# Kernel optimization log

Measured on AMD Instinct MI355X. Metric: run time of the kernel, lower is better.

The kernel has to match this reference:

```python
import jax, jax.numpy as jnp
import numpy as np

DIM = 1024
NUM_HEADS = 8
HEAD_DIM = 64
INNER = NUM_HEADS * HEAD_DIM  # 512


def setup_inputs() -> dict:
    key = jax.random.key(0)
    ks = jax.random.split(key, 7)
    B, N, M = 8, 512, 4096
    x = jax.random.normal(ks[0], (B, N, DIM), dtype=jnp.float32)
    context = jax.random.normal(ks[1], (B, M, DIM), dtype=jnp.float32)
    s_in = 1.0 / np.sqrt(DIM)
    s_inner = 1.0 / np.sqrt(INNER)
    # Linear weights stored as [in, out] for x @ W
    Wq = jax.random.normal(ks[2], (DIM, INNER), dtype=jnp.float32) * s_in
    Wk = jax.random.normal(ks[3], (DIM, INNER), dtype=jnp.float32) * s_in
    Wv = jax.random.normal(ks[4], (DIM, INNER), dtype=jnp.float32) * s_in
    Wo = jax.random.normal(ks[5], (INNER, DIM), dtype=jnp.float32) * s_inner
    bo = jax.random.normal(ks[6], (DIM,), dtype=jnp.float32) * 0.01
    return {"x": x, "context": context, "Wq": Wq, "Wk": Wk, "Wv": Wv, "Wo": Wo, "bo": bo}


def reference(x, context, Wq, Wk, Wv, Wo, bo):
    B, N, _ = x.shape
    M = context.shape[1]
    scale = HEAD_DIM ** -0.5
    # project and split heads: [B, H, N, D]
    q = (x @ Wq).reshape(B, N, NUM_HEADS, HEAD_DIM).transpose(0, 2, 1, 3)
    k = (context @ Wk).reshape(B, M, NUM_HEADS, HEAD_DIM).transpose(0, 2, 1, 3)
    v = (context @ Wv).reshape(B, M, NUM_HEADS, HEAD_DIM).transpose(0, 2, 1, 3)
    # full attention matrix [B, H, N, M] as in the original module
    attn = jax.nn.softmax(jnp.einsum('bhnd,bhmd->bhnm', q, k) * scale, axis=-1)
    out = jnp.einsum('bhnm,bhmd->bhnd', attn, v)  # [B, H, N, D]
    out = out.transpose(0, 2, 1, 3).reshape(B, N, INNER)
    return out @ Wo + bo
```

## Files before the change

kernel.cpp:

```cpp
#include <hip/hip_runtime.h>
#include <hip/hip_bf16.h>

#define B_SZ 8
#define N_Q 512
#define M_KV 4096
#define DIM 1024
#define INNER 512
#define NHEADS 8
#define HDIM 64

typedef __attribute__((ext_vector_type(4))) float floatx4;
typedef __attribute__((ext_vector_type(8))) short shortx8;
typedef __attribute__((ext_vector_type(4))) short shortx4;

__device__ inline unsigned short f2bf(float f) {
  union { float f; unsigned u; } x; x.f = f;
  unsigned r = x.u + 0x7FFFu + ((x.u >> 16) & 1u);
  return (unsigned short)(r >> 16);
}

__device__ inline shortx8 cvt8(floatx4 a, floatx4 b) {
  shortx8 h;
  h[0] = (short)f2bf(a[0]); h[1] = (short)f2bf(a[1]);
  h[2] = (short)f2bf(a[2]); h[3] = (short)f2bf(a[3]);
  h[4] = (short)f2bf(b[0]); h[5] = (short)f2bf(b[1]);
  h[6] = (short)f2bf(b[2]); h[7] = (short)f2bf(b[3]);
  return h;
}

__device__ inline void gload16(const void* g, void* l) {
  __builtin_amdgcn_global_load_lds(
      (const __attribute__((address_space(1))) void*)g,
      (__attribute__((address_space(3))) void*)l, 16, 0, 0);
}

__global__ void k_cvt_bf16(const float* __restrict__ src,
                           unsigned short* __restrict__ dst, long n) {
  long stride = (long)gridDim.x * 256 * 8;
  for (long i = ((long)blockIdx.x * 256 + threadIdx.x) * 8; i < n; i += stride) {
    floatx4 a = *reinterpret_cast<const floatx4*>(src + i);
    floatx4 b = *reinterpret_cast<const floatx4*>(src + i + 4);
    *reinterpret_cast<shortx8*>(dst + i) = cvt8(a, b);
  }
}

__global__ void k_transpose_all(const float* __restrict__ Wq,
                                const float* __restrict__ Wk,
                                const float* __restrict__ Wv,
                                const float* __restrict__ Wo,
                                unsigned short* __restrict__ Wqt,
                                unsigned short* __restrict__ Wkvt,
                                unsigned short* __restrict__ Wot) {
  __shared__ unsigned short t[32][36];
  const int z = blockIdx.z;
  const float* W;
  unsigned short* Wt;
  int K, N;
  if (z == 0)      { W = Wq; Wt = Wqt;  K = 1024; N = 512; }
  else if (z == 1) { W = Wk; Wt = Wkvt; K = 1024; N = 512; }
  else if (z == 2) { W = Wv; Wt = Wkvt + (size_t)512 * 1024; K = 1024; N = 512; }
  else             { W = Wo; Wt = Wot;  K = 512;  N = 1024; }
  if ((int)blockIdx.x * 32 >= K || (int)blockIdx.y * 32 >= N) return;
  const int kt = blockIdx.x * 32, nt = blockIdx.y * 32;
  const int tr = threadIdx.x >> 3;
  const int tc = (threadIdx.x & 7) * 4;
  floatx4 v = *reinterpret_cast<const floatx4*>(&W[(long)(kt + tr) * N + nt + tc]);
  #pragma unroll
  for (int j = 0; j < 4; ++j) t[tr][tc + j] = f2bf(v[j]);
  __syncthreads();
  shortx4 o;
  #pragma unroll
  for (int j = 0; j < 4; ++j) o[j] = (short)t[tc + j][tr];
  *reinterpret_cast<shortx4*>(&Wt[(long)(nt + tr) * K + kt + tc]) = o;
}

__global__ __launch_bounds__(256, 4)
void k_gemm_kv(const unsigned short* __restrict__ Ah,
               const unsigned short* __restrict__ Wkvt,
               unsigned short* __restrict__ Kh,
               unsigned short* __restrict__ Vt) {
  __shared__ unsigned short As[2][128 * 32];
  __shared__ unsigned short Bs[2][128 * 32];
  const int tid = threadIdx.x;
  const int lane = tid & 63;
  const int w = tid >> 6;
  const int wr = w >> 1, wc = w & 1;
  const int fr = lane & 15, fc = lane >> 4;

  const int L = ((blockIdx.x & 7) << 8) + (blockIdx.x >> 3);
  const int mt = L >> 3, nt = L & 7;
  const long arow0 = (long)mt << 7;
  const long bcol0 = (long)nt << 7;

  const int grow = lane >> 2;
  const int gpos = lane & 3;

  floatx4 acc[4][4] = {};

  #define STAGE(buf, kt)                                                      \
    {                                                                         \
      _Pragma("unroll")                                                       \
      for (int g = 0; g < 2; ++g) {                                           \
        const int rl = w * 32 + g * 16 + grow;                                \
        const int cc = gpos ^ ((rl >> 1) & 3);                                \
        gload16(Ah + (arow0 + rl) * 1024 + (kt) + cc * 8,                     \
                &As[buf][(w * 32 + g * 16) * 32]);                            \
        gload16(Wkvt + (bcol0 + rl) * 1024 + (kt) + cc * 8,                   \
                &Bs[buf][(w * 32 + g * 16) * 32]);                            \
      }                                                                       \
    }

  STAGE(0, 0);
  __syncthreads();

  for (int i = 0; i < 32; ++i) {
    const int cur = i & 1;
    if (i < 31) STAGE(cur ^ 1, (i + 1) << 5);

    shortx8 af[4], bf[4];
    #pragma unroll
    for (int rb = 0; rb < 4; ++rb) {
      int row = wr * 64 + rb * 16 + fr;
      af[rb] = *reinterpret_cast<const shortx8*>(
          &As[cur][row * 32 + ((fc ^ ((row >> 1) & 3)) * 8)]);
    }
    #pragma unroll
    for (int cb = 0; cb < 4; ++cb) {
      int row = wc * 64 + cb * 16 + fr;
      bf[cb] = *reinterpret_cast<const shortx8*>(
          &Bs[cur][row * 32 + ((fc ^ ((row >> 1) & 3)) * 8)]);
    }
    __builtin_amdgcn_s_setprio(1);
    #pragma unroll
    for (int rb = 0; rb < 4; ++rb) {
      #pragma unroll
      for (int cb = 0; cb < 4; ++cb)
        acc[rb][cb] = __builtin_amdgcn_mfma_f32_16x16x32_bf16(
            af[rb], bf[cb], acc[rb][cb], 0, 0, 0);
    }
    __builtin_amdgcn_s_setprio(0);
    __syncthreads();
  }
  #undef STAGE

  #pragma unroll
  for (int rb = 0; rb < 4; ++rb) {
    #pragma unroll
    for (int cb = 0; cb < 4; ++cb) {
      long gr0 = arow0 + wr * 64 + rb * 16 + fc * 4;
      long gc = bcol0 + wc * 64 + cb * 16 + fr;
      long b = gr0 >> 12, m = gr0 & 4095;
      if (gc < 512) {
        long h = gc >> 6, d = gc & 63;
        #pragma unroll
        for (int r = 0; r < 4; ++r)
          Kh[((((b * 8 + h) << 12) + m + r) << 6) + d] = f2bf(acc[rb][cb][r]);
      } else {
        long h = (gc - 512) >> 6, d = (gc - 512) & 63;
        shortx4 hv;
        #pragma unroll
        for (int r = 0; r < 4; ++r) hv[r] = (short)f2bf(acc[rb][cb][r]);
        *reinterpret_cast<shortx4*>(&Vt[(((b * 8 + h) * 64 + d) << 12) + m]) = hv;
      }
    }
  }
}

template<int MODE, bool ABF, int NCOL, int MBITS>
__global__ __launch_bounds__(512, 4)
void k_gemm(const void* __restrict__ Ap, const unsigned short* __restrict__ Bt,
            void* __restrict__ Cout, const float* __restrict__ bias,
            int M, int N, int K, float oscale) {
  __shared__ unsigned short As[2][128 * 32];
  __shared__ unsigned short Bs[2][256 * 32];
  const int tid = threadIdx.x;
  const int lane = tid & 63;
  const int w = tid >> 6;
  const int wr = w >> 2, wc = w & 3;

  const int cpx = gridDim.x >> 3;
  const int L = (blockIdx.x & 7) * cpx + (blockIdx.x >> 3);
  const long arow0 = (long)(L / NCOL) * 128;
  const long bcol0 = (long)(L % NCOL) * 256;

  const float* Af = (const float*)Ap;
  const unsigned short* Ah = (const unsigned short*)Ap;

  const int lsub = lane >> 2;
  const int lchunk = (lane & 3) ^ ((lane >> 3) & 3);
  const long brow0 = bcol0 + (w * 2 + 0) * 16 + lsub;
  const long brow1 = bcol0 + (w * 2 + 1) * 16 + lsub;
  const long ahrow = arow0 + w * 16 + lsub;
  const int arow = tid >> 2;
  const int acseg = tid & 3;
  const int aswz = arow * 32 + ((acseg ^ ((arow >> 1) & 3)) * 8);

  floatx4 acc[4][4] = {};

  #define STAGE_B(buf, kt)                                                   \
    {                                                                        \
      gload16(Bt + brow0 * K + (kt) + lchunk * 8, &Bs[buf][(w * 2) * 512]);  \
      gload16(Bt + brow1 * K + (kt) + lchunk * 8,                            \
              &Bs[buf][(w * 2 + 1) * 512]);                                  \
    }
  #define STAGE_AH(buf, kt) \
    gload16(Ah + ahrow * K + (kt) + lchunk * 8, &As[buf][w * 512]);

  if (ABF) {
    STAGE_AH(0, 0);
  } else {
    const float* src = Af + (arow0 + arow) * (long)K + acseg * 8;
    floatx4 a0 = *reinterpret_cast<const floatx4*>(src);
    floatx4 a1 = *reinterpret_cast<const floatx4*>(src + 4);
    *reinterpret_cast<shortx8*>(&As[0][aswz]) = cvt8(a0, a1);
  }
  STAGE_B(0, 0);
  __syncthreads();

  const int NK = K >> 5;
  for (int i = 0; i < NK; ++i) {
    const int cur = i & 1;
    const bool more = (i + 1) < NK;
    floatx4 a0, a1;
    if (more) {
      const long ktn = (long)(i + 1) << 5;
      if (ABF) {
        STAGE_AH(cur ^ 1, ktn);
      } else {
        const float* src = Af + (arow0 + arow) * (long)K + ktn + acseg * 8;
        a0 = *reinterpret_cast<const floatx4*>(src);
        a1 = *reinterpret_cast<const floatx4*>(src + 4);
      }
      STAGE_B(cur ^ 1, ktn);
    }

    shortx8 af[4], bf[4];
    #pragma unroll
    for (int rb = 0; rb < 4; ++rb) {
      int row = wr * 64 + rb * 16 + (lane & 15);
      af[rb] = *reinterpret_cast<const shortx8*>(
          &As[cur][row * 32 + (((lane >> 4) ^ ((row >> 1) & 3)) * 8)]);
    }
    #pragma unroll
    for (int cb = 0; cb < 4; ++cb) {
      int row = wc * 64 + cb * 16 + (lane & 15);
      bf[cb] = *reinterpret_cast<const shortx8*>(
          &Bs[cur][row * 32 + (((lane >> 4) ^ ((row >> 1) & 3)) * 8)]);
    }
    #pragma unroll
    for (int rb = 0; rb < 4; ++rb) {
      #pragma unroll
      for (int cb = 0; cb < 4; ++cb)
        acc[rb][cb] = __builtin_amdgcn_mfma_f32_16x16x32_bf16(
            af[rb], bf[cb], acc[rb][cb], 0, 0, 0);
    }

    if (more && !ABF)
      *reinterpret_cast<shortx8*>(&As[cur ^ 1][aswz]) = cvt8(a0, a1);
    __syncthreads();
  }
  #undef STAGE_B
  #undef STAGE_AH

  #pragma unroll
  for (int rb = 0; rb < 4; ++rb) {
    #pragma unroll
    for (int cb = 0; cb < 4; ++cb) {
      long gr0 = arow0 + wr * 64 + rb * 16 + (lane >> 4) * 4;
      long gc  = bcol0 + wc * 64 + cb * 16 + (lane & 15);
      if (MODE == 0) {
        float bv = bias[gc];
        #pragma unroll
        for (int r = 0; r < 4; ++r)
          ((float*)Cout)[(gr0 + r) * N + gc] = acc[rb][cb][r] + bv;
      } else if (MODE == 2) {
        long b = gr0 >> MBITS, m = gr0 & ((1 << MBITS) - 1);
        long h = gc >> 6, d = gc & 63;
        #pragma unroll
        for (int r = 0; r < 4; ++r)
          ((unsigned short*)Cout)[((((b * 8 + h) << MBITS) + m + r) << 6) + d] =
              f2bf(acc[rb][cb][r] * oscale);
      }
    }
  }
}

__global__ __launch_bounds__(256, 3)
void k_attn(const unsigned short* __restrict__ Qh,
            const unsigned short* __restrict__ Kh,
            const unsigned short* __restrict__ Vt,
            float* __restrict__ Opart, float* __restrict__ Lpart) {
  __shared__ unsigned short Qs[64 * 64];
  __shared__ unsigned short Ks[2][64 * 64];
  __shared__ unsigned short Vs[2][64 * 64];
  __shared__ unsigned short Ps[64][72];
  const int tid = threadIdx.x;
  const int lane = tid & 63;
  const int w = tid >> 6;
  const int wg = blockIdx.x;
  const int bh = wg & 63;
  const int qt = (wg >> 6) & 7;
  const int sp = wg >> 9;
  const int fr = lane & 15, fc = lane >> 4;

  const unsigned short* Qbase = Qh + (((long)bh << 9) + qt * 64) * 64;
  const unsigned short* Kbase = Kh + (((long)bh) << 18);
  const unsigned short* Vbase = Vt + (((long)bh) << 18);

  const int grow = lane >> 3;
  const int gpos = lane & 7;

  #define STAGE_KV(buf, mt_)                                              \
    { _Pragma("unroll")                                                   \
      for (int j = 0; j < 2; ++j) {                                       \
        const int r = w * 16 + j * 8 + grow;                              \
        const int c = gpos ^ (r & 7);                                     \
        gload16(Kbase + ((mt_) * 64 + r) * 64 + c * 8,                    \
                &Ks[buf][(w * 16 + j * 8) * 64]);                         \
        gload16(Vbase + (((long)r) << 12) + (mt_) * 64 + c * 8,           \
                &Vs[buf][(w * 16 + j * 8) * 64]);                         \
      } }

  const int mt0 = sp * 32;
  {
    #pragma unroll
    for (int j = 0; j < 2; ++j) {
      const int r = w * 16 + j * 8 + grow;
      const int c = gpos ^ (r & 7);
      gload16(Qbase + r * 64 + c * 8, &Qs[(w * 16 + j * 8) * 64]);
    }
    STAGE_KV(0, mt0);
  }
  __syncthreads();

  shortx8 qf[2];
  #pragma unroll
  for (int kk = 0; kk < 2; ++kk)
    qf[kk] = *reinterpret_cast<const shortx8*>(
        &Qs[(w * 16 + fr) * 64 + (((kk * 4 + fc) ^ (fr & 7)) * 8)]);

  floatx4 o_acc[4] = {};
  float l_part[4] = {0.f, 0.f, 0.f, 0.f};

  for (int it = 0; it < 32; ++it) {
    const int cur = it & 1;
    if (it < 31) STAGE_KV(cur ^ 1, mt0 + it + 1);

    floatx4 s[4];
    __builtin_amdgcn_s_setprio(1);
    #pragma unroll
    for (int cb = 0; cb < 4; ++cb) {
      int row = cb * 16 + fr;
      shortx8 k0 = *reinterpret_cast<const shortx8*>(
          &Ks[cur][row * 64 + ((fc ^ (fr & 7)) * 8)]);
      shortx8 k1 = *reinterpret_cast<const shortx8*>(
          &Ks[cur][row * 64 + (((4 + fc) ^ (fr & 7)) * 8)]);
      floatx4 z = {};
      z = __builtin_amdgcn_mfma_f32_16x16x32_bf16(qf[0], k0, z, 0, 0, 0);
      s[cb] = __builtin_amdgcn_mfma_f32_16x16x32_bf16(qf[1], k1, z, 0, 0, 0);
    }
    __builtin_amdgcn_s_setprio(0);

    #pragma unroll
    for (int cb = 0; cb < 4; ++cb) {
      #pragma unroll
      for (int r = 0; r < 4; ++r) {
        float pv = __expf(s[cb][r]);
        l_part[r] += pv;
        Ps[w * 16 + fc * 4 + r][cb * 16 + fr] = f2bf(pv);
      }
    }

    __builtin_amdgcn_s_setprio(1);
    #pragma unroll
    for (int kk = 0; kk < 2; ++kk) {
      shortx8 pf = *reinterpret_cast<const shortx8*>(
          &Ps[w * 16 + fr][kk * 32 + fc * 8]);
      #pragma unroll
      for (int db = 0; db < 4; ++db) {
        int row = db * 16 + fr;
        shortx8 vf = *reinterpret_cast<const shortx8*>(
            &Vs[cur][row * 64 + (((kk * 4 + fc) ^ (fr & 7)) * 8)]);
        o_acc[db] = __builtin_amdgcn_mfma_f32_16x16x32_bf16(
            pf, vf, o_acc[db], 0, 0, 0);
      }
    }
    __builtin_amdgcn_s_setprio(0);
    __syncthreads();
  }
  #undef STAGE_KV

  #pragma unroll
  for (int r = 0; r < 4; ++r) {
    float l = l_part[r];
    l += __shfl_xor(l, 1);
    l += __shfl_xor(l, 2);
    l += __shfl_xor(l, 4);
    l += __shfl_xor(l, 8);
    l_part[r] = l;
  }
  float* Ob = Opart + (long)wg * 4096;
  #pragma unroll
  for (int db = 0; db < 4; ++db) {
    #pragma unroll
    for (int r = 0; r < 4; ++r)
      Ob[(w * 16 + fc * 4 + r) * 64 + db * 16 + fr] = o_acc[db][r];
  }
  if (fr == 0) {
    #pragma unroll
    for (int r = 0; r < 4; ++r)
      Lpart[(long)wg * 64 + w * 16 + fc * 4 + r] = l_part[r];
  }
}

__global__ void k_attn_reduce(const float* __restrict__ Opart,
                              const float* __restrict__ Lpart,
                              unsigned short* __restrict__ Aat) {
  const int tid = threadIdx.x;
  const int g = blockIdx.x * 4 + (tid >> 6);
  const int d = tid & 63;
  const int bh = g >> 9, n = g & 511;
  const int b = bh >> 3, h = bh & 7;
  const int qt = n >> 6, rr = n & 63;
  const long i0 = ((long)(qt * 64 + bh)) * 4096 + rr * 64 + d;
  const long i1 = ((long)(512 + qt * 64 + bh)) * 4096 + rr * 64 + d;
  const float l = Lpart[(long)(qt * 64 + bh) * 64 + rr] +
                  Lpart[(long)(512 + qt * 64 + bh) * 64 + rr];
  const float o = Opart[i0] + Opart[i1];
  Aat[((long)(b * 512 + n)) * 512 + h * 64 + d] = f2bf(o / l);
}

extern "C" void kernel_launch(void* const* d_in, const int* in_sizes, int n_in,
                              void* d_out, int out_size, void* d_ws, size_t ws_size,
                              hipStream_t stream) {
  const float* x   = (const float*)d_in[0];
  const float* ctx = (const float*)d_in[1];
  const float* Wq  = (const float*)d_in[2];
  const float* Wk  = (const float*)d_in[3];
  const float* Wv  = (const float*)d_in[4];
  const float* Wo  = (const float*)d_in[5];
  const float* bo  = (const float*)d_in[6];
  float* out = (float*)d_out;

  char* ws = (char*)d_ws;
  unsigned short* Qh   = (unsigned short*)(ws);
  unsigned short* Kh   = (unsigned short*)(ws + (4ull  << 20));
  unsigned short* Vt   = (unsigned short*)(ws + (36ull << 20));
  unsigned short* ctxh = (unsigned short*)(ws + (68ull << 20));
  unsigned short* Aat  = (unsigned short*)(ws + (68ull << 20));
  float*          Opart= (float*)         (ws + (76ull << 20));
  float*          Lpart= (float*)         (ws + (92ull << 20));
  unsigned short* Wqt  = (unsigned short*)(ws + (132ull << 20));
  unsigned short* Wkvt = (unsigned short*)(ws + (133ull << 20));
  unsigned short* Wot  = (unsigned short*)(ws + (135ull << 20));

  k_cvt_bf16<<<dim3(2048), dim3(256), 0, stream>>>(
      ctx, ctxh, (long)B_SZ * M_KV * DIM);

  k_transpose_all<<<dim3(32, 32, 4), dim3(256), 0, stream>>>(
      Wq, Wk, Wv, Wo, Wqt, Wkvt, Wot);

  k_gemm<2, false, 2, 9><<<dim3(64), dim3(512), 0, stream>>>(
      x, Wqt, Qh, nullptr, B_SZ * N_Q, INNER, DIM, 0.125f);

  k_gemm_kv<<<dim3(2048), dim3(256), 0, stream>>>(ctxh, Wkvt, Kh, Vt);

  k_attn<<<dim3(1024), dim3(256), 0, stream>>>(Qh, Kh, Vt, Opart, Lpart);
  k_attn_reduce<<<dim3(8192), dim3(256), 0, stream>>>(Opart, Lpart, Aat);

  k_gemm<0, true, 4, 0><<<dim3(128), dim3(512), 0, stream>>>(
      Aat, Wot, out, bo, B_SZ * N_Q, DIM, INNER, 1.0f);
}
```

Baseline: 259.1 us.

## Fuse Q projection into KV GEMM, widen attention tiles, retile output GEMM

```diff
diff --git a/kernel.cpp b/kernel.cpp
--- a/kernel.cpp
+++ b/kernel.cpp
@@ -12,6 +12,8 @@
 typedef __attribute__((ext_vector_type(4))) float floatx4;
 typedef __attribute__((ext_vector_type(8))) short shortx8;
 typedef __attribute__((ext_vector_type(4))) short shortx4;
+
+#define QSCALE 0.18033688011112042f
 
 __device__ inline unsigned short f2bf(float f) {
   union { float f; unsigned u; } x; x.f = f;
@@ -75,47 +77,96 @@
 }
 
 __global__ __launch_bounds__(256, 4)
-void k_gemm_kv(const unsigned short* __restrict__ Ah,
-               const unsigned short* __restrict__ Wkvt,
-               unsigned short* __restrict__ Kh,
-               unsigned short* __restrict__ Vt) {
-  __shared__ unsigned short As[2][128 * 32];
-  __shared__ unsigned short Bs[2][128 * 32];
+void k_proj(const unsigned short* __restrict__ ctxh,
+            const float* __restrict__ x,
+            const unsigned short* __restrict__ Wkvt,
+            const unsigned short* __restrict__ Wqt,
+            unsigned short* __restrict__ Kh,
+            unsigned short* __restrict__ Vt,
+            unsigned short* __restrict__ Qh) {
+  __shared__ unsigned short As[2][4096];
+  __shared__ unsigned short Bs[2][4096];
   const int tid = threadIdx.x;
   const int lane = tid & 63;
   const int w = tid >> 6;
   const int wr = w >> 1, wc = w & 1;
   const int fr = lane & 15, fc = lane >> 4;
-
-  const int L = ((blockIdx.x & 7) << 8) + (blockIdx.x >> 3);
-  const int mt = L >> 3, nt = L & 7;
-  const long arow0 = (long)mt << 7;
-  const long bcol0 = (long)nt << 7;
+  const bool isQ = (int)blockIdx.x >= 2048;
+
+  long arow0, bcol0;
+  const unsigned short* Bb;
+  if (!isQ) {
+    const int L = ((blockIdx.x & 7) << 8) + (blockIdx.x >> 3);
+    arow0 = (long)(L >> 3) << 7;
+    bcol0 = (long)(L & 7) << 7;
+    Bb = Wkvt;
+  } else {
+    const int t = blockIdx.x - 2048;
+    arow0 = (long)(t >> 2) << 7;
+    bcol0 = (long)(t & 3) << 7;
+    Bb = Wqt;
+  }
 
   const int grow = lane >> 2;
   const int gpos = lane & 3;
+  const int arw = tid >> 1;
+  const int ahalf = tid & 1;
+  const int aswz = (arw >> 1) & 3;
+  const int as0 = ((2 * ahalf) ^ aswz) * 8;
+  const int as1 = ((2 * ahalf + 1) ^ aswz) * 8;
 
   floatx4 acc[4][4] = {};
 
-  #define STAGE(buf, kt)                                                      \
-    {                                                                         \
-      _Pragma("unroll")                                                       \
+  #define STAGE_A(buf, kt)                                                    \
+    { _Pragma("unroll")                                                       \
       for (int g = 0; g < 2; ++g) {                                           \
         const int rl = w * 32 + g * 16 + grow;                                \
         const int cc = gpos ^ ((rl >> 1) & 3);                                \
-        gload16(Ah + (arow0 + rl) * 1024 + (kt) + cc * 8,                     \
+        gload16(ctxh + (arow0 + rl) * 1024 + (kt) + cc * 8,                   \
                 &As[buf][(w * 32 + g * 16) * 32]);                            \
-        gload16(Wkvt + (bcol0 + rl) * 1024 + (kt) + cc * 8,                   \
+      } }
+  #define STAGE_B(buf, kt)                                                    \
+    { _Pragma("unroll")                                                       \
+      for (int g = 0; g < 2; ++g) {                                           \
+        const int rl = w * 32 + g * 16 + grow;                                \
+        const int cc = gpos ^ ((rl >> 1) & 3);                                \
+        gload16(Bb + (bcol0 + rl) * 1024 + (kt) + cc * 8,                     \
                 &Bs[buf][(w * 32 + g * 16) * 32]);                            \
-      }                                                                       \
-    }
-
-  STAGE(0, 0);
+      } }
+
+  if (!isQ) {
+    STAGE_A(0, 0);
+    STAGE_B(0, 0);
+  } else {
+    const float* s = x + (arow0 + arw) * 1024 + ahalf * 16;
+    floatx4 a0 = *reinterpret_cast<const floatx4*>(s);
+    floatx4 a1 = *reinterpret_cast<const floatx4*>(s + 4);
+    floatx4 a2 = *reinterpret_cast<const floatx4*>(s + 8);
+    floatx4 a3 = *reinterpret_cast<const floatx4*>(s + 12);
+    STAGE_B(0, 0);
+    *reinterpret_cast<shortx8*>(&As[0][arw * 32 + as0]) = cvt8(a0, a1);
+    *reinterpret_cast<shortx8*>(&As[0][arw * 32 + as1]) = cvt8(a2, a3);
+  }
   __syncthreads();
 
   for (int i = 0; i < 32; ++i) {
     const int cur = i & 1;
-    if (i < 31) STAGE(cur ^ 1, (i + 1) << 5);
+    const bool more = i < 31;
+    floatx4 a0, a1, a2, a3;
+    if (more) {
+      const int ktn = (i + 1) << 5;
+      if (!isQ) {
+        STAGE_A(cur ^ 1, ktn);
+        STAGE_B(cur ^ 1, ktn);
+      } else {
+        const float* s = x + (arow0 + arw) * 1024 + ktn + ahalf * 16;
+        a0 = *reinterpret_cast<const floatx4*>(s);
+        a1 = *reinterpret_cast<const floatx4*>(s + 4);
+        a2 = *reinterpret_cast<const floatx4*>(s + 8);
+        a3 = *reinterpret_cast<const floatx4*>(s + 12);
+        STAGE_B(cur ^ 1, ktn);
+      }
+    }
 
     shortx8 af[4], bf[4];
     #pragma unroll
@@ -139,9 +190,15 @@
             af[rb], bf[cb], acc[rb][cb], 0, 0, 0);
     }
     __builtin_amdgcn_s_setprio(0);
+
+    if (more && isQ) {
+      *reinterpret_cast<shortx8*>(&As[cur ^ 1][arw * 32 + as0]) = cvt8(a0, a1);
+      *reinterpret_cast<shortx8*>(&As[cur ^ 1][arw * 32 + as1]) = cvt8(a2, a3);
+    }
     __syncthreads();
   }
-  #undef STAGE
+  #undef STAGE_A
+  #undef STAGE_B
 
   #pragma unroll
   for (int rb = 0; rb < 4; ++rb) {
@@ -149,104 +206,85 @@
     for (int cb = 0; cb < 4; ++cb) {
       long gr0 = arow0 + wr * 64 + rb * 16 + fc * 4;
       long gc = bcol0 + wc * 64 + cb * 16 + fr;
-      long b = gr0 >> 12, m = gr0 & 4095;
-      if (gc < 512) {
+      if (!isQ) {
+        long b = gr0 >> 12, m = gr0 & 4095;
+        if (gc < 512) {
+          long h = gc >> 6, d = gc & 63;
+          #pragma unroll
+          for (int r = 0; r < 4; ++r)
+            Kh[((((b * 8 + h) << 12) + m + r) << 6) + d] = f2bf(acc[rb][cb][r]);
+        } else {
+          long h = (gc - 512) >> 6, d = (gc - 512) & 63;
+          shortx4 hv;
+          #pragma unroll
+          for (int r = 0; r < 4; ++r) hv[r] = (short)f2bf(acc[rb][cb][r]);
+          *reinterpret_cast<shortx4*>(&Vt[(((b * 8 + h) * 64 + d) << 12) + m]) = hv;
+        }
+      } else {
+        long b = gr0 >> 9, m = gr0 & 511;
         long h = gc >> 6, d = gc & 63;
         #pragma unroll
         for (int r = 0; r < 4; ++r)
-          Kh[((((b * 8 + h) << 12) + m + r) << 6) + d] = f2bf(acc[rb][cb][r]);
-      } else {
-        long h = (gc - 512) >> 6, d = (gc - 512) & 63;
-        shortx4 hv;
-        #pragma unroll
-        for (int r = 0; r < 4; ++r) hv[r] = (short)f2bf(acc[rb][cb][r]);
-        *reinterpret_cast<shortx4*>(&Vt[(((b * 8 + h) * 64 + d) << 12) + m]) = hv;
+          Qh[((((b * 8 + h) << 9) + m + r) << 6) + d] =
+              f2bf(acc[rb][cb][r] * QSCALE);
       }
     }
   }
 }
 
-template<int MODE, bool ABF, int NCOL, int MBITS>
-__global__ __launch_bounds__(512, 4)
-void k_gemm(const void* __restrict__ Ap, const unsigned short* __restrict__ Bt,
-            void* __restrict__ Cout, const float* __restrict__ bias,
-            int M, int N, int K, float oscale) {
-  __shared__ unsigned short As[2][128 * 32];
-  __shared__ unsigned short Bs[2][256 * 32];
+__global__ __launch_bounds__(256, 4)
+void k_out(const unsigned short* __restrict__ Aat,
+           const unsigned short* __restrict__ Wot,
+           float* __restrict__ out, const float* __restrict__ bias) {
+  __shared__ unsigned short As[2][4096];
+  __shared__ unsigned short Bs[2][4096];
   const int tid = threadIdx.x;
   const int lane = tid & 63;
   const int w = tid >> 6;
-  const int wr = w >> 2, wc = w & 3;
-
-  const int cpx = gridDim.x >> 3;
-  const int L = (blockIdx.x & 7) * cpx + (blockIdx.x >> 3);
-  const long arow0 = (long)(L / NCOL) * 128;
-  const long bcol0 = (long)(L % NCOL) * 256;
-
-  const float* Af = (const float*)Ap;
-  const unsigned short* Ah = (const unsigned short*)Ap;
-
-  const int lsub = lane >> 2;
-  const int lchunk = (lane & 3) ^ ((lane >> 3) & 3);
-  const long brow0 = bcol0 + (w * 2 + 0) * 16 + lsub;
-  const long brow1 = bcol0 + (w * 2 + 1) * 16 + lsub;
-  const long ahrow = arow0 + w * 16 + lsub;
-  const int arow = tid >> 2;
-  const int acseg = tid & 3;
-  const int aswz = arow * 32 + ((acseg ^ ((arow >> 1) & 3)) * 8);
+  const int wr = w >> 1, wc = w & 1;
+  const int fr = lane & 15, fc = lane >> 4;
+
+  const int L = ((blockIdx.x & 7) << 5) + (blockIdx.x >> 3);
+  const long arow0 = (long)(L >> 3) << 7;
+  const long bcol0 = (long)(L & 7) << 7;
+
+  const int grow = lane >> 2;
+  const int gpos = lane & 3;
 
   floatx4 acc[4][4] = {};
 
-  #define STAGE_B(buf, kt)                                                   \
-    {                                                                        \
-      gload16(Bt + brow0 * K + (kt) + lchunk * 8, &Bs[buf][(w * 2) * 512]);  \
-      gload16(Bt + brow1 * K + (kt) + lchunk * 8,                            \
-              &Bs[buf][(w * 2 + 1) * 512]);                                  \
-    }
-  #define STAGE_AH(buf, kt) \
-    gload16(Ah + ahrow * K + (kt) + lchunk * 8, &As[buf][w * 512]);
-
-  if (ABF) {
-    STAGE_AH(0, 0);
-  } else {
-    const float* src = Af + (arow0 + arow) * (long)K + acseg * 8;
-    floatx4 a0 = *reinterpret_cast<const floatx4*>(src);
-    floatx4 a1 = *reinterpret_cast<const floatx4*>(src + 4);
-    *reinterpret_cast<shortx8*>(&As[0][aswz]) = cvt8(a0, a1);
-  }
-  STAGE_B(0, 0);
+  #define STAGE2(buf, kt)                                                     \
+    { _Pragma("unroll")                                                       \
+      for (int g = 0; g < 2; ++g) {                                           \
+        const int rl = w * 32 + g * 16 + grow;                                \
+        const int cc = gpos ^ ((rl >> 1) & 3);                                \
+        gload16(Aat + (arow0 + rl) * 512 + (kt) + cc * 8,                     \
+                &As[buf][(w * 32 + g * 16) * 32]);                            \
+        gload16(Wot + (bcol0 + rl) * 512 + (kt) + cc * 8,                     \
+                &Bs[buf][(w * 32 + g * 16) * 32]);                            \
+      } }
+
+  STAGE2(0, 0);
   __syncthreads();
 
-  const int NK = K >> 5;
-  for (int i = 0; i < NK; ++i) {
+  for (int i = 0; i < 16; ++i) {
     const int cur = i & 1;
-    const bool more = (i + 1) < NK;
-    floatx4 a0, a1;
-    if (more) {
-      const long ktn = (long)(i + 1) << 5;
-      if (ABF) {
-        STAGE_AH(cur ^ 1, ktn);
-      } else {
-        const float* src = Af + (arow0 + arow) * (long)K + ktn + acseg * 8;
-        a0 = *reinterpret_cast<const floatx4*>(src);
-        a1 = *reinterpret_cast<const floatx4*>(src + 4);
-      }
-      STAGE_B(cur ^ 1, ktn);
-    }
+    if (i < 15) STAGE2(cur ^ 1, (i + 1) << 5);
 
     shortx8 af[4], bf[4];
     #pragma unroll
     for (int rb = 0; rb < 4; ++rb) {
-      int row = wr * 64 + rb * 16 + (lane & 15);
+      int row = wr * 64 + rb * 16 + fr;
       af[rb] = *reinterpret_cast<const shortx8*>(
-          &As[cur][row * 32 + (((lane >> 4) ^ ((row >> 1) & 3)) * 8)]);
+          &As[cur][row * 32 + ((fc ^ ((row >> 1) & 3)) * 8)]);
     }
     #pragma unroll
     for (int cb = 0; cb < 4; ++cb) {
-      int row = wc * 64 + cb * 16 + (lane & 15);
+      int row = wc * 64 + cb * 16 + fr;
       bf[cb] = *reinterpret_cast<const shortx8*>(
-          &Bs[cur][row * 32 + (((lane >> 4) ^ ((row >> 1) & 3)) * 8)]);
-    }
+          &Bs[cur][row * 32 + ((fc ^ ((row >> 1) & 3)) * 8)]);
+    }
+    __builtin_amdgcn_s_setprio(1);
     #pragma unroll
     for (int rb = 0; rb < 4; ++rb) {
       #pragma unroll
@@ -254,33 +292,21 @@
         acc[rb][cb] = __builtin_amdgcn_mfma_f32_16x16x32_bf16(
             af[rb], bf[cb], acc[rb][cb], 0, 0, 0);
     }
-
-    if (more && !ABF)
-      *reinterpret_cast<shortx8*>(&As[cur ^ 1][aswz]) = cvt8(a0, a1);
+    __builtin_amdgcn_s_setprio(0);
     __syncthreads();
   }
-  #undef STAGE_B
-  #undef STAGE_AH
+  #undef STAGE2
 
   #pragma unroll
   for (int rb = 0; rb < 4; ++rb) {
     #pragma unroll
     for (int cb = 0; cb < 4; ++cb) {
-      long gr0 = arow0 + wr * 64 + rb * 16 + (lane >> 4) * 4;
-      long gc  = bcol0 + wc * 64 + cb * 16 + (lane & 15);
-      if (MODE == 0) {
-        float bv = bias[gc];
-        #pragma unroll
-        for (int r = 0; r < 4; ++r)
-          ((float*)Cout)[(gr0 + r) * N + gc] = acc[rb][cb][r] + bv;
-      } else if (MODE == 2) {
-        long b = gr0 >> MBITS, m = gr0 & ((1 << MBITS) - 1);
-        long h = gc >> 6, d = gc & 63;
-        #pragma unroll
-        for (int r = 0; r < 4; ++r)
-          ((unsigned short*)Cout)[((((b * 8 + h) << MBITS) + m + r) << 6) + d] =
-              f2bf(acc[rb][cb][r] * oscale);
-      }
+      long gr0 = arow0 + wr * 64 + rb * 16 + fc * 4;
+      long gc = bcol0 + wc * 64 + cb * 16 + fr;
+      float bv = bias[gc];
+      #pragma unroll
+      for (int r = 0; r < 4; ++r)
+        out[(gr0 + r) * 1024 + gc] = acc[rb][cb][r] + bv;
     }
   }
 }
@@ -290,20 +316,19 @@
             const unsigned short* __restrict__ Kh,
             const unsigned short* __restrict__ Vt,
             float* __restrict__ Opart, float* __restrict__ Lpart) {
-  __shared__ unsigned short Qs[64 * 64];
   __shared__ unsigned short Ks[2][64 * 64];
   __shared__ unsigned short Vs[2][64 * 64];
-  __shared__ unsigned short Ps[64][72];
+  __shared__ unsigned short QPs[128 * 72];
   const int tid = threadIdx.x;
   const int lane = tid & 63;
   const int w = tid >> 6;
   const int wg = blockIdx.x;
   const int bh = wg & 63;
-  const int qt = (wg >> 6) & 7;
-  const int sp = wg >> 9;
+  const int qt = (wg >> 6) & 3;
+  const int sp = wg >> 8;
   const int fr = lane & 15, fc = lane >> 4;
 
-  const unsigned short* Qbase = Qh + (((long)bh << 9) + qt * 64) * 64;
+  const unsigned short* Qbase = Qh + (((long)bh << 9) + qt * 128) * 64;
   const unsigned short* Kbase = Kh + (((long)bh) << 18);
   const unsigned short* Vbase = Vt + (((long)bh) << 18);
 
@@ -321,68 +346,85 @@
                 &Vs[buf][(w * 16 + j * 8) * 64]);                         \
       } }
 
-  const int mt0 = sp * 32;
+  const int mt0 = sp * 16;
   {
     #pragma unroll
-    for (int j = 0; j < 2; ++j) {
-      const int r = w * 16 + j * 8 + grow;
+    for (int j = 0; j < 4; ++j) {
+      const int r = w * 32 + j * 8 + grow;
       const int c = gpos ^ (r & 7);
-      gload16(Qbase + r * 64 + c * 8, &Qs[(w * 16 + j * 8) * 64]);
+      gload16(Qbase + r * 64 + c * 8, &QPs[(w * 32 + j * 8) * 64]);
     }
     STAGE_KV(0, mt0);
   }
   __syncthreads();
 
-  shortx8 qf[2];
-  #pragma unroll
-  for (int kk = 0; kk < 2; ++kk)
-    qf[kk] = *reinterpret_cast<const shortx8*>(
-        &Qs[(w * 16 + fr) * 64 + (((kk * 4 + fc) ^ (fr & 7)) * 8)]);
-
-  floatx4 o_acc[4] = {};
-  float l_part[4] = {0.f, 0.f, 0.f, 0.f};
-
-  for (int it = 0; it < 32; ++it) {
+  shortx8 qf[2][2];
+  #pragma unroll
+  for (int rf = 0; rf < 2; ++rf) {
+    const int row = w * 32 + rf * 16 + fr;
+    #pragma unroll
+    for (int kk = 0; kk < 2; ++kk)
+      qf[rf][kk] = *reinterpret_cast<const shortx8*>(
+          &QPs[row * 64 + (((kk * 4 + fc) ^ (row & 7)) * 8)]);
+  }
+  __syncthreads();
+
+  floatx4 o_acc[2][4] = {};
+  float l_part[2][4] = {};
+
+  for (int it = 0; it < 16; ++it) {
     const int cur = it & 1;
-    if (it < 31) STAGE_KV(cur ^ 1, mt0 + it + 1);
-
-    floatx4 s[4];
+    if (it < 15) STAGE_KV(cur ^ 1, mt0 + it + 1);
+
+    floatx4 s[2][4];
     __builtin_amdgcn_s_setprio(1);
     #pragma unroll
     for (int cb = 0; cb < 4; ++cb) {
-      int row = cb * 16 + fr;
+      const int krow = cb * 16 + fr;
       shortx8 k0 = *reinterpret_cast<const shortx8*>(
-          &Ks[cur][row * 64 + ((fc ^ (fr & 7)) * 8)]);
+          &Ks[cur][krow * 64 + ((fc ^ (fr & 7)) * 8)]);
       shortx8 k1 = *reinterpret_cast<const shortx8*>(
-          &Ks[cur][row * 64 + (((4 + fc) ^ (fr & 7)) * 8)]);
-      floatx4 z = {};
-      z = __builtin_amdgcn_mfma_f32_16x16x32_bf16(qf[0], k0, z, 0, 0, 0);
-      s[cb] = __builtin_amdgcn_mfma_f32_16x16x32_bf16(qf[1], k1, z, 0, 0, 0);
+          &Ks[cur][krow * 64 + (((4 + fc) ^ (fr & 7)) * 8)]);
+      #pragma unroll
+      for (int rf = 0; rf < 2; ++rf) {
+        floatx4 z = {};
+        z = __builtin_amdgcn_mfma_f32_16x16x32_bf16(qf[rf][0], k0, z, 0, 0, 0);
+        s[rf][cb] = __builtin_amdgcn_mfma_f32_16x16x32_bf16(
+            qf[rf][1], k1, z, 0, 0, 0);
+      }
     }
     __builtin_amdgcn_s_setprio(0);
 
     #pragma unroll
-    for (int cb = 0; cb < 4; ++cb) {
-      #pragma unroll
-      for (int r = 0; r < 4; ++r) {
-        float pv = __expf(s[cb][r]);
-        l_part[r] += pv;
-        Ps[w * 16 + fc * 4 + r][cb * 16 + fr] = f2bf(pv);
+    for (int rf = 0; rf < 2; ++rf) {
+      #pragma unroll
+      for (int cb = 0; cb < 4; ++cb) {
+        #pragma unroll
+        for (int r = 0; r < 4; ++r) {
+          float pv = exp2f(s[rf][cb][r]);
+          l_part[rf][r] += pv;
+          QPs[(w * 32 + rf * 16 + fc * 4 + r) * 72 + cb * 16 + fr] = f2bf(pv);
+        }
       }
     }
 
     __builtin_amdgcn_s_setprio(1);
     #pragma unroll
     for (int kk = 0; kk < 2; ++kk) {
-      shortx8 pf = *reinterpret_cast<const shortx8*>(
-          &Ps[w * 16 + fr][kk * 32 + fc * 8]);
+      shortx8 pf[2];
+      #pragma unroll
+      for (int rf = 0; rf < 2; ++rf)
+        pf[rf] = *reinterpret_cast<const shortx8*>(
+            &QPs[(w * 32 + rf * 16 + fr) * 72 + kk * 32 + fc * 8]);
       #pragma unroll
       for (int db = 0; db < 4; ++db) {
-        int row = db * 16 + fr;
+        const int vrow = db * 16 + fr;
         shortx8 vf = *reinterpret_cast<const shortx8*>(
-            &Vs[cur][row * 64 + (((kk * 4 + fc) ^ (fr & 7)) * 8)]);
-        o_acc[db] = __builtin_amdgcn_mfma_f32_16x16x32_bf16(
-            pf, vf, o_acc[db], 0, 0, 0);
+            &Vs[cur][vrow * 64 + (((kk * 4 + fc) ^ (fr & 7)) * 8)]);
+        #pragma unroll
+        for (int rf = 0; rf < 2; ++rf)
+          o_acc[rf][db] = __builtin_amdgcn_mfma_f32_16x16x32_bf16(
+              pf[rf], vf, o_acc[rf][db], 0, 0, 0);
       }
     }
     __builtin_amdgcn_s_setprio(0);
@@ -390,26 +432,22 @@
   }
   #undef STAGE_KV
 
-  #pragma unroll
-  for (int r = 0; r < 4; ++r) {
-    float l = l_part[r];
-    l += __shfl_xor(l, 1);
-    l += __shfl_xor(l, 2);
-    l += __shfl_xor(l, 4);
-    l += __shfl_xor(l, 8);
-    l_part[r] = l;
-  }
-  float* Ob = Opart + (long)wg * 4096;
-  #pragma unroll
-  for (int db = 0; db < 4; ++db) {
-    #pragma unroll
-    for (int r = 0; r < 4; ++r)
-      Ob[(w * 16 + fc * 4 + r) * 64 + db * 16 + fr] = o_acc[db][r];
-  }
-  if (fr == 0) {
-    #pragma unroll
-    for (int r = 0; r < 4; ++r)
-      Lpart[(long)wg * 64 + w * 16 + fc * 4 + r] = l_part[r];
+  float* Ob = Opart + (long)wg * 8192;
+  #pragma unroll
+  for (int rf = 0; rf < 2; ++rf) {
+    #pragma unroll
+    for (int r = 0; r < 4; ++r) {
+      float l = l_part[rf][r];
+      l += __shfl_xor(l, 1);
+      l += __shfl_xor(l, 2);
+      l += __shfl_xor(l, 4);
+      l += __shfl_xor(l, 8);
+      const int prow = w * 32 + rf * 16 + fc * 4 + r;
+      if (fr == 0) Lpart[(long)wg * 128 + prow] = l;
+      #pragma unroll
+      for (int db = 0; db < 4; ++db)
+        Ob[prow * 64 + db * 16 + fr] = o_acc[rf][db][r];
+    }
   }
 }
 
@@ -421,12 +459,14 @@
   const int d = tid & 63;
   const int bh = g >> 9, n = g & 511;
   const int b = bh >> 3, h = bh & 7;
-  const int qt = n >> 6, rr = n & 63;
-  const long i0 = ((long)(qt * 64 + bh)) * 4096 + rr * 64 + d;
-  const long i1 = ((long)(512 + qt * 64 + bh)) * 4096 + rr * 64 + d;
-  const float l = Lpart[(long)(qt * 64 + bh) * 64 + rr] +
-                  Lpart[(long)(512 + qt * 64 + bh) * 64 + rr];
-  const float o = Opart[i0] + Opart[i1];
+  const int qt = n >> 7, rr = n & 127;
+  float o = 0.f, l = 0.f;
+  #pragma unroll
+  for (int p = 0; p < 4; ++p) {
+    const long wgp = ((p * 4 + qt) << 6) + bh;
+    o += Opart[wgp * 8192 + rr * 64 + d];
+    l += Lpart[wgp * 128 + rr];
+  }
   Aat[((long)(b * 512 + n)) * 512 + h * 64 + d] = f2bf(o / l);
 }
 
@@ -449,7 +489,7 @@
   unsigned short* ctxh = (unsigned short*)(ws + (68ull << 20));
   unsigned short* Aat  = (unsigned short*)(ws + (68ull << 20));
   float*          Opart= (float*)         (ws + (76ull << 20));
-  float*          Lpart= (float*)         (ws + (92ull << 20));
+  float*          Lpart= (float*)         (ws + (110ull << 20));
   unsigned short* Wqt  = (unsigned short*)(ws + (132ull << 20));
   unsigned short* Wkvt = (unsigned short*)(ws + (133ull << 20));
   unsigned short* Wot  = (unsigned short*)(ws + (135ull << 20));
@@ -460,14 +500,11 @@
   k_transpose_all<<<dim3(32, 32, 4), dim3(256), 0, stream>>>(
       Wq, Wk, Wv, Wo, Wqt, Wkvt, Wot);
 
-  k_gemm<2, false, 2, 9><<<dim3(64), dim3(512), 0, stream>>>(
-      x, Wqt, Qh, nullptr, B_SZ * N_Q, INNER, DIM, 0.125f);
-
-  k_gemm_kv<<<dim3(2048), dim3(256), 0, stream>>>(ctxh, Wkvt, Kh, Vt);
+  k_proj<<<dim3(2176), dim3(256), 0, stream>>>(
+      ctxh, x, Wkvt, Wqt, Kh, Vt, Qh);
 
   k_attn<<<dim3(1024), dim3(256), 0, stream>>>(Qh, Kh, Vt, Opart, Lpart);
   k_attn_reduce<<<dim3(8192), dim3(256), 0, stream>>>(Opart, Lpart, Aat);
 
-  k_gemm<0, true, 4, 0><<<dim3(128), dim3(512), 0, stream>>>(
-      Aat, Wot, out, bo, B_SZ * N_Q, DIM, INNER, 1.0f);
-}
+  k_out<<<dim3(256), dim3(256), 0, stream>>>(Aat, Wot, out, bo);
+}
```

New measurement: 244.4 us. 1.06x faster.
